# Kernel optimization log

Measured on AMD Instinct MI355X. Metric: run time of the kernel, lower is better.

## Reference

```python
import jax, jax.numpy as jnp
import numpy as np

B, N, DIM, H = 2, 2048, 1024, 16
D = DIM // H  # head_dim = 64


def setup_inputs() -> dict:
    key = jax.random.key(0)
    ks = jax.random.split(key, 3)
    w_scale = 0.02
    return {
        "x": jax.random.normal(ks[0], (B, N, DIM), dtype=jnp.float32),
        "Wqkv": jax.random.normal(ks[1], (DIM, 3 * DIM), dtype=jnp.float32) * w_scale,
        "bqkv": jnp.zeros((3 * DIM,), dtype=jnp.float32),
        "Wproj": jax.random.normal(ks[2], (DIM, DIM), dtype=jnp.float32) * w_scale,
        "bproj": jnp.zeros((DIM,), dtype=jnp.float32),
        "sigma": jnp.ones((1,), dtype=jnp.float32),
        "gamma": jnp.ones((1,), dtype=jnp.float32),
    }


def reference(x, Wqkv, bqkv, Wproj, bproj, sigma, gamma):
    b, n, c = x.shape
    # qkv projection -> (B, N, 3, H, D)
    qkv = (x @ Wqkv + bqkv).reshape(b, n, 3, H, D)
    q = jnp.transpose(qkv[:, :, 0], (0, 2, 1, 3))  # [B, H, N, D]
    k = jnp.transpose(qkv[:, :, 1], (0, 2, 1, 3))
    v = jnp.transpose(qkv[:, :, 2], (0, 2, 1, 3))
    scale = 1.0 / jnp.sqrt(jnp.asarray(D, dtype=x.dtype))
    scores = jnp.einsum("bhqd,bhkd->bhqk", q, k) * scale  # [B, H, N, N]
    # divisive normalization (cortical gain control) over key axis
    denom = sigma + jnp.sqrt(jnp.mean(scores * scores, axis=-1, keepdims=True))
    scores = gamma * scores / denom
    attn = jax.nn.softmax(scores, axis=-1)
    out = jnp.einsum("bhqk,bhkd->bhqd", attn, v)  # [B, H, N, D]
    out = jnp.transpose(out, (0, 2, 1, 3)).reshape(b, n, c)
    return out @ Wproj + bproj
```

## Files before the change

kernel.cpp:

```cpp
#include <hip/hip_runtime.h>

typedef __attribute__((ext_vector_type(4))) float f32x4;
typedef __attribute__((ext_vector_type(8))) _Float16 f16x8;
typedef __attribute__((ext_vector_type(4))) _Float16 f16x4;
typedef __attribute__((ext_vector_type(2))) _Float16 f16x2;

#define MFMA_F16(a, b, c) __builtin_amdgcn_mfma_f32_16x16x32_f16(a, b, c, 0, 0, 0)

__device__ __forceinline__ void gload_lds16(const void* g, void* l) {
  __builtin_amdgcn_global_load_lds(
      (const __attribute__((address_space(1))) void*)g,
      (__attribute__((address_space(3))) void*)l, 16, 0, 0);
}
__device__ __forceinline__ f16x2 pk2(float a, float b) {
  return __builtin_bit_cast(f16x2, __builtin_amdgcn_cvt_pkrtz(a, b));
}
__device__ __forceinline__ void pipe_barrier_v4() {
  asm volatile("s_waitcnt vmcnt(4) lgkmcnt(0)" ::: "memory");
  __builtin_amdgcn_sched_barrier(0);
  __builtin_amdgcn_s_barrier();
}
__device__ __forceinline__ void pipe_barrier_v0() {
  asm volatile("s_waitcnt vmcnt(0) lgkmcnt(0)" ::: "memory");
  __builtin_amdgcn_sched_barrier(0);
  __builtin_amdgcn_s_barrier();
}

__global__ __launch_bounds__(256) void cast_x_kernel(
    const float* __restrict__ x, _Float16* __restrict__ xf, int n4) {
  int i = blockIdx.x * 256 + threadIdx.x;
  if (i >= n4) return;
  f32x4 v = *(const f32x4*)(x + (size_t)i * 4);
  f16x4 h;
#pragma unroll
  for (int j = 0; j < 4; ++j) h[j] = (_Float16)v[j];
  *(f16x4*)(xf + (size_t)i * 4) = h;
}

__global__ __launch_bounds__(256) void transpose_w_kernel(
    const float* __restrict__ W, _Float16* __restrict__ wt, int K, int N) {
  __shared__ float tile[32][33];
  const int n0 = blockIdx.x * 32, k0 = blockIdx.y * 32;
  const int tx = threadIdx.x & 31, ty = threadIdx.x >> 5;
#pragma unroll
  for (int j = 0; j < 32; j += 8)
    tile[ty + j][tx] = W[(size_t)(k0 + ty + j) * N + n0 + tx];
  __syncthreads();
#pragma unroll
  for (int j = 0; j < 32; j += 8)
    wt[(size_t)(n0 + ty + j) * K + k0 + tx] = (_Float16)tile[tx][ty + j];
}

__global__ __launch_bounds__(256) void gemm_qkv_kernel(
    const _Float16* __restrict__ xf, const _Float16* __restrict__ wt,
    const float* __restrict__ bias, _Float16* __restrict__ QF,
    _Float16* __restrict__ KF, _Float16* __restrict__ KT,
    _Float16* __restrict__ VT) {
  __shared__ __attribute__((aligned(16))) _Float16 lg[24576];
  const int tid = threadIdx.x, lane = tid & 63, w = tid >> 6;
  const int m0 = blockIdx.y * 128, n0 = blockIdx.x * 128;
  const int wr = (w >> 1) * 64, wc = (w & 1) * 64;
  f32x4 acc[4][4] = {};

  const int srow = lane >> 2;
  const int scol = (((lane & 3) ^ ((lane >> 3) & 3)) * 8);
  const int fr = lane & 15, fg = lane >> 4;
  const int rswz = (fr >> 1) & 3;

  auto stageT = [&](int buf, int k0) {
#pragma unroll
    for (int j = 0; j < 2; ++j) {
      const int rbase = 32 * w + 16 * j;
      const int r = rbase + srow;
      gload_lds16(xf + (size_t)(m0 + r) * 1024 + k0 + scol,
                  &lg[buf * 8192 + rbase * 32]);
      gload_lds16(wt + (size_t)(n0 + r) * 1024 + k0 + scol,
                  &lg[buf * 8192 + 4096 + rbase * 32]);
    }
  };

  stageT(0, 0);
  stageT(1, 32);
  pipe_barrier_v4();
  int cur = 0;
  for (int t = 0; t < 32; ++t) {
    if (t < 30) {
      const int nb = (cur + 2 >= 3) ? cur - 1 : cur + 2;
      stageT(nb, (t + 2) * 32);
    }
    const int ab = cur * 8192;
    f16x8 af[4], bfr[4];
#pragma unroll
    for (int m = 0; m < 4; ++m)
      af[m] = *(const f16x8*)&lg[ab + (wr + 16 * m + fr) * 32 + ((fg ^ rswz) * 8)];
#pragma unroll
    for (int n = 0; n < 4; ++n)
      bfr[n] = *(const f16x8*)&lg[ab + 4096 + (wc + 16 * n + fr) * 32 + ((fg ^ rswz) * 8)];
#pragma unroll
    for (int m = 0; m < 4; ++m)
#pragma unroll
      for (int n = 0; n < 4; ++n) acc[m][n] = MFMA_F16(af[m], bfr[n], acc[m][n]);
    if (t < 30) pipe_barrier_v4(); else pipe_barrier_v0();
    cur = (cur + 1 == 3) ? 0 : cur + 1;
  }

  const int fq = fg * 4;
#pragma unroll
  for (int n = 0; n < 4; ++n) {
    const float bv = bias[n0 + wc + 16 * n + fr];
#pragma unroll
    for (int m = 0; m < 4; ++m)
#pragma unroll
      for (int i = 0; i < 4; ++i)
        lg[(wr + 16 * m + fq + i) * 129 + wc + 16 * n + fr] =
            (_Float16)(acc[m][n][i] + bv);
  }
  __syncthreads();
  const int b = m0 >> 11, nnb = m0 & 2047;
  const int h0 = 2 * (blockIdx.x & 7);
  const int sPhase = blockIdx.x >> 3;
  if (sPhase <= 1) {
    _Float16* __restrict__ dst = (sPhase == 0) ? QF : KF;
#pragma unroll
    for (int p = 0; p < 8; ++p) {
      const int r = p * 16 + (tid >> 4);
      const int c = tid & 15;
      f16x8 vals;
#pragma unroll
      for (int j = 0; j < 8; ++j) vals[j] = lg[r * 129 + c * 8 + j];
      const int h = c >> 3, d = (c & 7) * 8;
      *(f16x8*)&dst[((size_t)((b * 16 + h0 + h) * 2048 + nnb + r)) * 64 + d] = vals;
    }
  }
  if (sPhase >= 1) {
    _Float16* __restrict__ T = (sPhase == 1) ? KT : VT;
#pragma unroll
    for (int p = 0; p < 8; ++p) {
      const int lr = p * 16 + (tid >> 4);
      const int cc = tid & 15;
      f16x8 vals;
#pragma unroll
      for (int j = 0; j < 8; ++j) vals[j] = lg[(cc * 8 + j) * 129 + lr];
      const int h = lr >> 6, d = lr & 63;
      *(f16x8*)&T[((size_t)((b * 16 + h0 + h) * 64 + d)) * 2048 + nnb + cc * 8] = vals;
    }
  }
}

__global__ __launch_bounds__(256) void gram_kernel(
    const _Float16* __restrict__ KT, _Float16* __restrict__ GH,
    _Float16* __restrict__ GL) {
  __shared__ __attribute__((aligned(16))) _Float16 sT[2][4096];
  const int tid = threadIdx.x, lane = tid & 63, w = tid >> 6;
  const int bh = blockIdx.x;
  const _Float16* src = KT + (size_t)bh * 64 * 2048;
  const int s_r = lane >> 3, s_cg = lane & 7;
  const int fr = lane & 15, fg = lane >> 4;
  const int kswz = fr & 7;

  auto stage = [&](int buf, int n0) {
#pragma unroll
    for (int j = 0; j < 2; ++j) {
      const int rbase = 8 * w + 32 * j;
      gload_lds16(src + (size_t)(rbase + s_r) * 2048 + n0 + ((s_cg ^ s_r) * 8),
                  &sT[buf][rbase * 64]);
    }
  };

  f32x4 acc[4] = {};
  stage(0, 0);
  __syncthreads();
  for (int t = 0; t < 32; ++t) {
    const int cur = t & 1;
    if (t < 31) stage(cur ^ 1, (t + 1) * 64);
    f16x8 af[2];
#pragma unroll
    for (int ks = 0; ks < 2; ++ks)
      af[ks] = *(const f16x8*)&sT[cur][(16 * w + fr) * 64 + (((ks * 4 + fg) ^ kswz) * 8)];
#pragma unroll
    for (int nt = 0; nt < 4; ++nt)
#pragma unroll
      for (int ks = 0; ks < 2; ++ks)
        acc[nt] = MFMA_F16(
            af[ks],
            *(const f16x8*)&sT[cur][(16 * nt + fr) * 64 + (((ks * 4 + fg) ^ kswz) * 8)],
            acc[nt]);
    __syncthreads();
  }
#pragma unroll
  for (int nt = 0; nt < 4; ++nt) {
#pragma unroll
    for (int i = 0; i < 4; ++i) {
      const float g = acc[nt][i];
      const _Float16 gh = (_Float16)g;
      const size_t o = (size_t)bh * 4096 + (16 * w + fg * 4 + i) * 64 + 16 * nt + fr;
      GH[o] = gh;
      GL[o] = (_Float16)(g - (float)gh);
    }
  }
}

__global__ __launch_bounds__(256) void attn_kernel(
    const _Float16* __restrict__ QF, const _Float16* __restrict__ KF,
    const _Float16* __restrict__ VT, const _Float16* __restrict__ GH,
    const _Float16* __restrict__ GL, _Float16* __restrict__ OB,
    const float* __restrict__ sigma_p, const float* __restrict__ gamma_p) {
  __shared__ __attribute__((aligned(16))) _Float16 lds[24576];

  const int tid = threadIdx.x, lane = tid & 63, w = tid >> 6;
  const int bh = blockIdx.y;
  const int q0 = blockIdx.x * 128;
  const size_t base = (size_t)bh * (2048 * 64);
  const float sigma = sigma_p[0], gamma = gamma_p[0];
  const int fr = lane & 15, fg = lane >> 4;
  const int s_r = lane >> 3, s_cg = lane & 7;
  const int kswz = fr & 7;

  const _Float16* Kbh = KF + base;
  const _Float16* Tbh = VT + base;

  f16x8 qf[2][2];
#pragma unroll
  for (int m = 0; m < 2; ++m)
#pragma unroll
    for (int ks = 0; ks < 2; ++ks)
      qf[m][ks] = *(const f16x8*)(QF + base +
                                  (size_t)(q0 + 32 * w + 16 * m + fr) * 64 +
                                  ks * 32 + fg * 8);

  auto stage64 = [&](int dstoff, const _Float16* g, int srcstride) {
#pragma unroll
    for (int j = 0; j < 2; ++j) {
      const int rbase = 8 * w + 32 * j;
      gload_lds16(g + (size_t)(rbase + s_r) * srcstride + ((s_cg ^ s_r) * 8),
                  &lds[dstoff + rbase * 64]);
    }
  };
  auto stage64K = [&](int dstoff, const _Float16* g) {
#pragma unroll
    for (int j = 0; j < 2; ++j) {
      const int rbase = 8 * w + 32 * j;
      const int r = rbase + s_r;
      const int pr = (r & 0x23) | ((r & 0x0C) << 1) | ((r & 0x10) >> 2);
      gload_lds16(g + (size_t)pr * 64 + ((s_cg ^ s_r) * 8),
                  &lds[dstoff + rbase * 64]);
    }
  };

  stage64(0, GH + (size_t)bh * 4096, 64);
  stage64(4096, GL + (size_t)bh * 4096, 64);
  __syncthreads();
  float minvl2[2];
  float* Yp = (float*)&lds[8192 + w * 2048];
#pragma unroll
  for (int m = 0; m < 2; ++m) {
    f32x4 yacc[4] = {};
#pragma unroll
    for (int nt = 0; nt < 4; ++nt) {
#pragma unroll
      for (int ks = 0; ks < 2; ++ks) {
        const int off = (16 * nt + fr) * 64 + (((ks * 4 + fg) ^ kswz) * 8);
        yacc[nt] = MFMA_F16(qf[m][ks], *(const f16x8*)&lds[off], yacc[nt]);
        yacc[nt] = MFMA_F16(qf[m][ks], *(const f16x8*)&lds[4096 + off], yacc[nt]);
      }
    }
#pragma unroll
    for (int nt = 0; nt < 4; ++nt)
#pragma unroll
      for (int i = 0; i < 4; ++i) Yp[(fg * 4 + i) * 64 + 16 * nt + fr] = yacc[nt][i];
    float zp = 0.0f;
#pragma unroll
    for (int ks = 0; ks < 2; ++ks) {
      const f32x4 y0 = *(const f32x4*)&Yp[fr * 64 + ks * 32 + fg * 8];
      const f32x4 y1 = *(const f32x4*)&Yp[fr * 64 + ks * 32 + fg * 8 + 4];
#pragma unroll
      for (int c = 0; c < 4; ++c) {
        zp += y0[c] * (float)qf[m][ks][c];
        zp += y1[c] * (float)qf[m][ks][c + 4];
      }
    }
    zp += __shfl_xor(zp, 16);
    zp += __shfl_xor(zp, 32);
    const float rms = sqrtf(fmaxf(zp, 0.0f)) * (1.0f / 362.038672f);
    minvl2[m] = gamma / (sigma + rms) * 0.125f * 1.44269504f;
  }
  __syncthreads();

  float lsum[2] = {};
  f32x4 oacc[2][4] = {};
  stage64K(0, Kbh);
  stage64(12288, Tbh, 2048);
  stage64K(4096, Kbh + 64 * 64);
  stage64(16384, Tbh + 64, 2048);
  pipe_barrier_v4();
  int cur = 0;
  for (int kb = 0; kb < 32; ++kb) {
    if (kb < 30) {
      const int nb = (cur + 2 >= 3) ? cur - 1 : cur + 2;
      stage64K(nb * 4096, Kbh + (size_t)(kb + 2) * 64 * 64);
      stage64(12288 + nb * 4096, Tbh + (kb + 2) * 64, 2048);
    }
    const int koff = cur * 4096, voff = 12288 + cur * 4096;
    f32x4 pacc[2][4];
#pragma unroll
    for (int n = 0; n < 4; ++n) {
      const int offb = koff + (16 * n + fr) * 64;
      const f16x8 kf0 = *(const f16x8*)&lds[offb + ((fg ^ kswz) * 8)];
      const f16x8 kf1 = *(const f16x8*)&lds[offb + (((4 + fg) ^ kswz) * 8)];
#pragma unroll
      for (int m = 0; m < 2; ++m) {
        f32x4 a = {};
        a = MFMA_F16(kf0, qf[m][0], a);
        a = MFMA_F16(kf1, qf[m][1], a);
        pacc[m][n] = a;
      }
    }
#pragma unroll
    for (int m = 0; m < 2; ++m)
#pragma unroll
      for (int n = 0; n < 4; ++n)
#pragma unroll
        for (int i = 0; i < 4; ++i) {
          const float p = __builtin_amdgcn_exp2f(pacc[m][n][i] * minvl2[m]);
          lsum[m] += p;
          pacc[m][n][i] = p;
        }
#pragma unroll
    for (int ks2 = 0; ks2 < 2; ++ks2) {
      f16x8 bf[2];
#pragma unroll
      for (int m = 0; m < 2; ++m) {
        const f16x2 c0 = pk2(pacc[m][2 * ks2][0], pacc[m][2 * ks2][1]);
        const f16x2 c1 = pk2(pacc[m][2 * ks2][2], pacc[m][2 * ks2][3]);
        const f16x2 c2 = pk2(pacc[m][2 * ks2 + 1][0], pacc[m][2 * ks2 + 1][1]);
        const f16x2 c3 = pk2(pacc[m][2 * ks2 + 1][2], pacc[m][2 * ks2 + 1][3]);
        bf[m][0] = c0[0]; bf[m][1] = c0[1]; bf[m][2] = c1[0]; bf[m][3] = c1[1];
        bf[m][4] = c2[0]; bf[m][5] = c2[1]; bf[m][6] = c3[0]; bf[m][7] = c3[1];
      }
#pragma unroll
      for (int nf = 0; nf < 4; ++nf) {
        const int off = voff + (16 * nf + fr) * 64 + (((ks2 * 4 + fg) ^ kswz) * 8);
        const f16x8 vt = *(const f16x8*)&lds[off];
        oacc[0][nf] = MFMA_F16(vt, bf[0], oacc[0][nf]);
        oacc[1][nf] = MFMA_F16(vt, bf[1], oacc[1][nf]);
      }
    }
    if (kb < 30) pipe_barrier_v4(); else pipe_barrier_v0();
    cur = (cur + 1 == 3) ? 0 : cur + 1;
  }
  float inv[2];
#pragma unroll
  for (int m = 0; m < 2; ++m) {
    lsum[m] += __shfl_xor(lsum[m], 16);
    lsum[m] += __shfl_xor(lsum[m], 32);
    inv[m] = 1.0f / lsum[m];
  }

  const int b = bh >> 4, h = bh & 15;
#pragma unroll
  for (int m = 0; m < 2; ++m) {
    const size_t orow = (size_t)(b * 2048 + q0 + 32 * w + 16 * m + fr);
#pragma unroll
    for (int nf = 0; nf < 4; ++nf) {
      f16x4 ov;
#pragma unroll
      for (int i = 0; i < 4; ++i) ov[i] = (_Float16)(oacc[m][nf][i] * inv[m]);
      *(f16x4*)&OB[orow * 1024 + h * 64 + 16 * nf + 4 * fg] = ov;
    }
  }
}

__global__ __launch_bounds__(256) void gemm_proj_kernel(
    const _Float16* __restrict__ A, const _Float16* __restrict__ Bt,
    const float* __restrict__ bias, float* __restrict__ out) {
  __shared__ __attribute__((aligned(16))) _Float16 lg[24576];
  const int tid = threadIdx.x, lane = tid & 63, w = tid >> 6;
  const int m0 = blockIdx.y * 128, n0 = blockIdx.x * 128;
  const int wr = (w >> 1) * 64, wc = (w & 1) * 64;
  f32x4 acc[4][4] = {};
  const int srow = lane >> 2;
  const int scol = (((lane & 3) ^ ((lane >> 3) & 3)) * 8);
  const int fr = lane & 15, fg = lane >> 4;
  const int rswz = (fr >> 1) & 3;

  auto stageT = [&](int buf, int k0) {
#pragma unroll
    for (int j = 0; j < 2; ++j) {
      const int rbase = 32 * w + 16 * j;
      const int r = rbase + srow;
      gload_lds16(A + (size_t)(m0 + r) * 1024 + k0 + scol,
                  &lg[buf * 8192 + rbase * 32]);
      gload_lds16(Bt + (size_t)(n0 + r) * 1024 + k0 + scol,
                  &lg[buf * 8192 + 4096 + rbase * 32]);
    }
  };

  stageT(0, 0);
  stageT(1, 32);
  pipe_barrier_v4();
  int cur = 0;
  for (int t = 0; t < 32; ++t) {
    if (t < 30) {
      const int nb = (cur + 2 >= 3) ? cur - 1 : cur + 2;
      stageT(nb, (t + 2) * 32);
    }
    const int ab = cur * 8192;
    f16x8 af[4], bfr[4];
#pragma unroll
    for (int m = 0; m < 4; ++m)
      af[m] = *(const f16x8*)&lg[ab + (wr + 16 * m + fr) * 32 + ((fg ^ rswz) * 8)];
#pragma unroll
    for (int n = 0; n < 4; ++n)
      bfr[n] = *(const f16x8*)&lg[ab + 4096 + (wc + 16 * n + fr) * 32 + ((fg ^ rswz) * 8)];
#pragma unroll
    for (int m = 0; m < 4; ++m)
#pragma unroll
      for (int n = 0; n < 4; ++n) acc[m][n] = MFMA_F16(af[m], bfr[n], acc[m][n]);
    if (t < 30) pipe_barrier_v4(); else pipe_barrier_v0();
    cur = (cur + 1 == 3) ? 0 : cur + 1;
  }
  const int fq = fg * 4;
#pragma unroll
  for (int n = 0; n < 4; ++n) {
    const int col = n0 + wc + 16 * n + fr;
    const float bv = bias[col];
#pragma unroll
    for (int m = 0; m < 4; ++m) {
#pragma unroll
      for (int i = 0; i < 4; ++i) {
        const int row = m0 + wr + 16 * m + fq + i;
        out[(size_t)row * 1024 + col] = acc[m][n][i] + bv;
      }
    }
  }
}

extern "C" void kernel_launch(void* const* d_in, const int* in_sizes, int n_in,
                              void* d_out, int out_size, void* d_ws, size_t ws_size,
                              hipStream_t stream) {
  const float* x = (const float*)d_in[0];
  const float* Wqkv = (const float*)d_in[1];
  const float* bqkv = (const float*)d_in[2];
  const float* Wproj = (const float*)d_in[3];
  const float* bproj = (const float*)d_in[4];
  const float* sigma = (const float*)d_in[5];
  const float* gamma = (const float*)d_in[6];
  float* out = (float*)d_out;

  char* ws = (char*)d_ws;
  const size_t MB = 1024 * 1024;
  _Float16* XF  = (_Float16*)(ws + 0 * MB);
  _Float16* WQT = (_Float16*)(ws + 8 * MB);
  _Float16* WPT = (_Float16*)(ws + 14 * MB);
  _Float16* QF  = (_Float16*)(ws + 16 * MB);
  _Float16* KF  = (_Float16*)(ws + 24 * MB);
  _Float16* VT  = (_Float16*)(ws + 32 * MB);
  _Float16* KT  = (_Float16*)(ws + 40 * MB);
  _Float16* OB  = (_Float16*)(ws + 40 * MB);
  _Float16* GH  = (_Float16*)(ws + 8 * MB);
  _Float16* GL  = (_Float16*)(ws + 8 * MB + 512 * 1024);

  cast_x_kernel<<<4096, 256, 0, stream>>>(x, XF, 1048576);
  transpose_w_kernel<<<dim3(96, 32), 256, 0, stream>>>(Wqkv, WQT, 1024, 3072);
  transpose_w_kernel<<<dim3(32, 32), 256, 0, stream>>>(Wproj, WPT, 1024, 1024);
  gemm_qkv_kernel<<<dim3(24, 32), 256, 0, stream>>>(XF, WQT, bqkv, QF, KF, KT, VT);
  gram_kernel<<<32, 256, 0, stream>>>(KT, GH, GL);
  attn_kernel<<<dim3(16, 32), 256, 0, stream>>>(QF, KF, VT, GH, GL, OB, sigma, gamma);
  gemm_proj_kernel<<<dim3(8, 32), 256, 0, stream>>>(OB, WPT, bproj, out);
}
```

Measured before the change: 133.7 us.

## Fuse prep kernels, remap blocks for XCD L2 locality, triple-buffer gram loads

Merges the cast and two weight-transpose kernels into one launch to cut launch overhead. Switches the GEMM, attention and projection grids to 1D and remaps block indices so that blocks sharing the same operand tiles or heads land on the same XCD (blockIdx mod 8), aiming for better L2 reuse. Converts the gram kernel to a three-stage LDS pipeline with partial vmcnt waits so it overlaps global loads with MFMA work. The remapping adds index arithmetic and depends on the assumed round-robin dispatch of blocks across XCDs.

Measured after the change: 126.2 us. 1.06x faster.

```diff
diff --git a/kernel.cpp b/kernel.cpp
--- a/kernel.cpp
+++ b/kernel.cpp
@@ -20,27 +20,44 @@
   __builtin_amdgcn_sched_barrier(0);
   __builtin_amdgcn_s_barrier();
 }
+__device__ __forceinline__ void pipe_barrier_v2() {
+  asm volatile("s_waitcnt vmcnt(2) lgkmcnt(0)" ::: "memory");
+  __builtin_amdgcn_sched_barrier(0);
+  __builtin_amdgcn_s_barrier();
+}
 __device__ __forceinline__ void pipe_barrier_v0() {
   asm volatile("s_waitcnt vmcnt(0) lgkmcnt(0)" ::: "memory");
   __builtin_amdgcn_sched_barrier(0);
   __builtin_amdgcn_s_barrier();
 }
 
-__global__ __launch_bounds__(256) void cast_x_kernel(
-    const float* __restrict__ x, _Float16* __restrict__ xf, int n4) {
-  int i = blockIdx.x * 256 + threadIdx.x;
-  if (i >= n4) return;
-  f32x4 v = *(const f32x4*)(x + (size_t)i * 4);
-  f16x4 h;
-#pragma unroll
-  for (int j = 0; j < 4; ++j) h[j] = (_Float16)v[j];
-  *(f16x4*)(xf + (size_t)i * 4) = h;
-}
-
-__global__ __launch_bounds__(256) void transpose_w_kernel(
-    const float* __restrict__ W, _Float16* __restrict__ wt, int K, int N) {
+__global__ __launch_bounds__(256) void prep_kernel(
+    const float* __restrict__ x, _Float16* __restrict__ xf,
+    const float* __restrict__ Wqkv, _Float16* __restrict__ wqt,
+    const float* __restrict__ Wproj, _Float16* __restrict__ wpt) {
   __shared__ float tile[32][33];
-  const int n0 = blockIdx.x * 32, k0 = blockIdx.y * 32;
+  const int bx = blockIdx.x;
+  if (bx < 4096) {
+    const int i = bx * 256 + threadIdx.x;
+    f32x4 v = *(const f32x4*)(x + (size_t)i * 4);
+    f16x4 h;
+#pragma unroll
+    for (int j = 0; j < 4; ++j) h[j] = (_Float16)v[j];
+    *(f16x4*)(xf + (size_t)i * 4) = h;
+    return;
+  }
+  const float* W;
+  _Float16* wt;
+  int N, n0, k0;
+  if (bx < 7168) {
+    const int t = bx - 4096;
+    W = Wqkv; wt = wqt; N = 3072;
+    n0 = (t % 96) * 32; k0 = (t / 96) * 32;
+  } else {
+    const int t = bx - 7168;
+    W = Wproj; wt = wpt; N = 1024;
+    n0 = (t % 32) * 32; k0 = (t / 32) * 32;
+  }
   const int tx = threadIdx.x & 31, ty = threadIdx.x >> 5;
 #pragma unroll
   for (int j = 0; j < 32; j += 8)
@@ -48,7 +65,7 @@
   __syncthreads();
 #pragma unroll
   for (int j = 0; j < 32; j += 8)
-    wt[(size_t)(n0 + ty + j) * K + k0 + tx] = (_Float16)tile[tx][ty + j];
+    wt[(size_t)(n0 + ty + j) * 1024 + k0 + tx] = (_Float16)tile[tx][ty + j];
 }
 
 __global__ __launch_bounds__(256) void gemm_qkv_kernel(
@@ -58,7 +75,11 @@
     _Float16* __restrict__ VT) {
   __shared__ __attribute__((aligned(16))) _Float16 lg[24576];
   const int tid = threadIdx.x, lane = tid & 63, w = tid >> 6;
-  const int m0 = blockIdx.y * 128, n0 = blockIdx.x * 128;
+  const int wg = blockIdx.x;
+  const int cx = wg & 7, c = wg >> 3;
+  const int bxl = (cx & 1) * 12 + c % 12;
+  const int byl = (cx >> 1) * 8 + c / 12;
+  const int m0 = byl * 128, n0 = bxl * 128;
   const int wr = (w >> 1) * 64, wc = (w & 1) * 64;
   f32x4 acc[4][4] = {};
 
@@ -117,18 +138,18 @@
   }
   __syncthreads();
   const int b = m0 >> 11, nnb = m0 & 2047;
-  const int h0 = 2 * (blockIdx.x & 7);
-  const int sPhase = blockIdx.x >> 3;
+  const int h0 = 2 * (bxl & 7);
+  const int sPhase = bxl >> 3;
   if (sPhase <= 1) {
     _Float16* __restrict__ dst = (sPhase == 0) ? QF : KF;
 #pragma unroll
     for (int p = 0; p < 8; ++p) {
       const int r = p * 16 + (tid >> 4);
-      const int c = tid & 15;
+      const int cc = tid & 15;
       f16x8 vals;
 #pragma unroll
-      for (int j = 0; j < 8; ++j) vals[j] = lg[r * 129 + c * 8 + j];
-      const int h = c >> 3, d = (c & 7) * 8;
+      for (int j = 0; j < 8; ++j) vals[j] = lg[r * 129 + cc * 8 + j];
+      const int h = cc >> 3, d = (cc & 7) * 8;
       *(f16x8*)&dst[((size_t)((b * 16 + h0 + h) * 2048 + nnb + r)) * 64 + d] = vals;
     }
   }
@@ -150,7 +171,7 @@
 __global__ __launch_bounds__(256) void gram_kernel(
     const _Float16* __restrict__ KT, _Float16* __restrict__ GH,
     _Float16* __restrict__ GL) {
-  __shared__ __attribute__((aligned(16))) _Float16 sT[2][4096];
+  __shared__ __attribute__((aligned(16))) _Float16 sT[3][4096];
   const int tid = threadIdx.x, lane = tid & 63, w = tid >> 6;
   const int bh = blockIdx.x;
   const _Float16* src = KT + (size_t)bh * 64 * 2048;
@@ -169,10 +190,14 @@
 
   f32x4 acc[4] = {};
   stage(0, 0);
-  __syncthreads();
+  stage(1, 64);
+  pipe_barrier_v2();
+  int cur = 0;
   for (int t = 0; t < 32; ++t) {
-    const int cur = t & 1;
-    if (t < 31) stage(cur ^ 1, (t + 1) * 64);
+    if (t < 30) {
+      const int nb = (cur + 2 >= 3) ? cur - 1 : cur + 2;
+      stage(nb, (t + 2) * 64);
+    }
     f16x8 af[2];
 #pragma unroll
     for (int ks = 0; ks < 2; ++ks)
@@ -185,7 +210,8 @@
             af[ks],
             *(const f16x8*)&sT[cur][(16 * nt + fr) * 64 + (((ks * 4 + fg) ^ kswz) * 8)],
             acc[nt]);
-    __syncthreads();
+    if (t < 30) pipe_barrier_v2(); else pipe_barrier_v0();
+    cur = (cur + 1 == 3) ? 0 : cur + 1;
   }
 #pragma unroll
   for (int nt = 0; nt < 4; ++nt) {
@@ -208,8 +234,10 @@
   __shared__ __attribute__((aligned(16))) _Float16 lds[24576];
 
   const int tid = threadIdx.x, lane = tid & 63, w = tid >> 6;
-  const int bh = blockIdx.y;
-  const int q0 = blockIdx.x * 128;
+  const int wg = blockIdx.x;
+  const int c = wg >> 3;
+  const int bh = (wg & 7) * 4 + (c >> 4);
+  const int q0 = (c & 15) * 128;
   const size_t base = (size_t)bh * (2048 * 64);
   const float sigma = sigma_p[0], gamma = gamma_p[0];
   const int fr = lane & 15, fg = lane >> 4;
@@ -274,9 +302,9 @@
       const f32x4 y0 = *(const f32x4*)&Yp[fr * 64 + ks * 32 + fg * 8];
       const f32x4 y1 = *(const f32x4*)&Yp[fr * 64 + ks * 32 + fg * 8 + 4];
 #pragma unroll
-      for (int c = 0; c < 4; ++c) {
-        zp += y0[c] * (float)qf[m][ks][c];
-        zp += y1[c] * (float)qf[m][ks][c + 4];
+      for (int cc = 0; cc < 4; ++cc) {
+        zp += y0[cc] * (float)qf[m][ks][cc];
+        zp += y1[cc] * (float)qf[m][ks][cc + 4];
       }
     }
     zp += __shfl_xor(zp, 16);
@@ -375,7 +403,11 @@
     const float* __restrict__ bias, float* __restrict__ out) {
   __shared__ __attribute__((aligned(16))) _Float16 lg[24576];
   const int tid = threadIdx.x, lane = tid & 63, w = tid >> 6;
-  const int m0 = blockIdx.y * 128, n0 = blockIdx.x * 128;
+  const int wg = blockIdx.x;
+  const int c = wg >> 3;
+  const int bxl = c & 7;
+  const int byl = (wg & 7) * 4 + (c >> 3);
+  const int m0 = byl * 128, n0 = bxl * 128;
   const int wr = (w >> 1) * 64, wc = (w & 1) * 64;
   f32x4 acc[4][4] = {};
   const int srow = lane >> 2;
@@ -460,11 +492,9 @@
   _Float16* GH  = (_Float16*)(ws + 8 * MB);
   _Float16* GL  = (_Float16*)(ws + 8 * MB + 512 * 1024);
 
-  cast_x_kernel<<<4096, 256, 0, stream>>>(x, XF, 1048576);
-  transpose_w_kernel<<<dim3(96, 32), 256, 0, stream>>>(Wqkv, WQT, 1024, 3072);
-  transpose_w_kernel<<<dim3(32, 32), 256, 0, stream>>>(Wproj, WPT, 1024, 1024);
-  gemm_qkv_kernel<<<dim3(24, 32), 256, 0, stream>>>(XF, WQT, bqkv, QF, KF, KT, VT);
+  prep_kernel<<<8192, 256, 0, stream>>>(x, XF, Wqkv, WQT, Wproj, WPT);
+  gemm_qkv_kernel<<<768, 256, 0, stream>>>(XF, WQT, bqkv, QF, KF, KT, VT);
   gram_kernel<<<32, 256, 0, stream>>>(KT, GH, GL);
-  attn_kernel<<<dim3(16, 32), 256, 0, stream>>>(QF, KF, VT, GH, GL, OB, sigma, gamma);
-  gemm_proj_kernel<<<dim3(8, 32), 256, 0, stream>>>(OB, WPT, bproj, out);
-}
+  attn_kernel<<<512, 256, 0, stream>>>(QF, KF, VT, GH, GL, OB, sigma, gamma);
+  gemm_proj_kernel<<<256, 256, 0, stream>>>(OB, WPT, bproj, out);
+}
```
